# Performance work log

Measured on AMD Instinct MI355X. Metric: run time of the kernel, lower is better.

Reference implementation:

```python
import jax, jax.numpy as jnp
import numpy as np

N_EMBD = 2048
N_HEAD = 16
HEAD_DIM = N_EMBD // N_HEAD
MAX_SEQ = 2048
ROPE_BASE = 10000.0


def _build_rope_cache(seq_len, head_dim, base):
    theta = 1.0 / (base ** (jnp.arange(0, head_dim, 2, dtype=jnp.float32) / head_dim))
    idx_theta = jnp.arange(seq_len, dtype=jnp.float32)[:, None] * theta[None, :]  # [T, hd/2]
    return jnp.cos(idx_theta), jnp.sin(idx_theta)


def _apply_rope(x, cos, sin):
    # x: [B, T, H, hd]; interleaved (even, odd) pairing along last dim
    B, T, H, hd = x.shape
    xf = x.astype(jnp.float32).reshape(B, T, H, hd // 2, 2)
    x0, x1 = xf[..., 0], xf[..., 1]
    c = cos[None, :T, None, :]
    s = sin[None, :T, None, :]
    out = jnp.stack([x0 * c - x1 * s, x1 * c + x0 * s], axis=-1)
    return out.reshape(B, T, H, hd).astype(x.dtype)


def setup_inputs() -> dict:
    key = jax.random.key(0)
    k1, k2, k3 = jax.random.split(key, 3)
    x = jax.random.normal(k1, (2, 2048, N_EMBD), dtype=jnp.float32)
    # torch Linear(D, 3D, bias=False): y = x @ W.T ; store as [D, 3D] for x @ W
    scale = 1.0 / np.sqrt(N_EMBD)
    w_attn = jax.random.normal(k2, (N_EMBD, 3 * N_EMBD), dtype=jnp.float32) * scale
    w_proj = jax.random.normal(k3, (N_EMBD, N_EMBD), dtype=jnp.float32) * scale
    return {"x": x, "w_attn": w_attn, "w_proj": w_proj}


def reference(x, w_attn, w_proj):
    B, T, D = x.shape
    cos, sin = _build_rope_cache(MAX_SEQ, HEAD_DIM, ROPE_BASE)
    qkv = x @ w_attn                                   # [B, T, 3D]
    q, k, v = jnp.split(qkv, 3, axis=-1)
    q = q.reshape(B, T, N_HEAD, HEAD_DIM)
    k = k.reshape(B, T, N_HEAD, HEAD_DIM)
    v = v.reshape(B, T, N_HEAD, HEAD_DIM)
    q = _apply_rope(q, cos, sin)
    k = _apply_rope(k, cos, sin)
    # non-causal SDPA (original calls F.sdpa without is_causal)
    scale = 1.0 / jnp.sqrt(jnp.asarray(HEAD_DIM, dtype=q.dtype))
    scores = jnp.einsum("bqhd,bkhd->bhqk", q, k) * scale
    attn = jax.nn.softmax(scores, axis=-1)
    y = jnp.einsum("bhqk,bkhd->bqhd", attn, v).reshape(B, T, D)
    return y @ w_proj
```

## Files before the change

kernel.cpp:

```cpp
#include <hip/hip_runtime.h>
#include <cstdint>
#include <cstddef>

typedef __attribute__((ext_vector_type(8))) short bf16x8;
typedef __attribute__((ext_vector_type(8))) unsigned short us8;
typedef __attribute__((ext_vector_type(4))) float f32x4;

#define TSEQ 2048

__device__ __forceinline__ unsigned short f2bf(float f) {
  union { float f; uint32_t u; } v; v.f = f;
  uint32_t u = v.u;
  uint32_t r = (u + 0x7FFFu + ((u >> 16) & 1u)) >> 16;
  return (unsigned short)r;
}
__device__ __forceinline__ unsigned short f2bf_trunc(float f) {
  union { float f; uint32_t u; } v; v.f = f;
  return (unsigned short)(v.u >> 16);
}
__device__ __forceinline__ float bf2f(unsigned short h) {
  union { uint32_t u; float f; } v; v.u = ((uint32_t)h) << 16;
  return v.f;
}

__device__ __forceinline__ void async16(const void* g, void* l) {
  __builtin_amdgcn_global_load_lds(
      (const __attribute__((address_space(1))) unsigned int*)g,
      (__attribute__((address_space(3))) unsigned int*)l,
      16, 0, 0);
}

__global__ __launch_bounds__(256) void cvt_x(
    const float* __restrict__ in, unsigned short* __restrict__ out)
{
  const size_t i = ((size_t)blockIdx.x * 256 + threadIdx.x) * 16;
  f32x4 a0 = *(const f32x4*)(in + i);
  f32x4 a1 = *(const f32x4*)(in + i + 4);
  f32x4 a2 = *(const f32x4*)(in + i + 8);
  f32x4 a3 = *(const f32x4*)(in + i + 12);
  us8 lo, hi;
#pragma unroll
  for (int j = 0; j < 4; j++) {
    lo[j] = f2bf(a0[j]); lo[j + 4] = f2bf(a1[j]);
    hi[j] = f2bf(a2[j]); hi[j + 4] = f2bf(a3[j]);
  }
  *(us8*)(out + i) = lo;
  *(us8*)(out + i + 8) = hi;
}

__global__ __launch_bounds__(256) void transpose_w(
    const float* __restrict__ in, unsigned short* __restrict__ out,
    int R, int C)
{
  __shared__ unsigned short tile[32][33];
  const int bx = blockIdx.x * 32;
  const int by = blockIdx.y * 32;
  const int tx = threadIdx.x & 31;
  const int ty = threadIdx.x >> 5;
#pragma unroll
  for (int r = ty; r < 32; r += 8)
    tile[r][tx] = f2bf(in[(size_t)(by + r) * C + bx + tx]);
  __syncthreads();
#pragma unroll
  for (int r = ty; r < 32; r += 8)
    out[(size_t)(bx + r) * R + by + tx] = tile[tx][r];
}

template <int CF32>
__global__ __launch_bounds__(256) void gemm_bt(
    const unsigned short* __restrict__ A,
    const unsigned short* __restrict__ Bt,
    void* __restrict__ Cv,
    int M, int N, int K, int ldc)
{
  __shared__ unsigned short As[2][128 * 32];
  __shared__ unsigned short Bs[2][128 * 32];
  const int tid  = threadIdx.x;
  const int lane = tid & 63;
  const int w    = tid >> 6;
  const int m0   = blockIdx.y * 128;
  const int n0   = blockIdx.x * 128;
  const int wm   = (w & 1) * 64;
  const int wn   = (w >> 1) * 64;

  const int srow = lane >> 2;
  const int scol = (lane & 3) * 8;
  const unsigned short* ga0 = A  + (size_t)(m0 + w * 16 + srow) * K + scol;
  const unsigned short* ga1 = ga0 + (size_t)64 * K;
  const unsigned short* gb0 = Bt + (size_t)(n0 + w * 16 + srow) * K + scol;
  const unsigned short* gb1 = gb0 + (size_t)64 * K;

  f32x4 acc[4][4];
#pragma unroll
  for (int i = 0; i < 4; i++)
#pragma unroll
    for (int j = 0; j < 4; j++) acc[i][j] = (f32x4){0.f, 0.f, 0.f, 0.f};

  const int frow = lane & 15;
  const int fcol = (lane >> 4) * 8;

  for (int kt = 0; kt < K; kt += 64) {
    __syncthreads();
    async16(ga0 + kt,      &As[0][w * 512]);
    async16(ga1 + kt,      &As[0][(4 + w) * 512]);
    async16(ga0 + kt + 32, &As[1][w * 512]);
    async16(ga1 + kt + 32, &As[1][(4 + w) * 512]);
    async16(gb0 + kt,      &Bs[0][w * 512]);
    async16(gb1 + kt,      &Bs[0][(4 + w) * 512]);
    async16(gb0 + kt + 32, &Bs[1][w * 512]);
    async16(gb1 + kt + 32, &Bs[1][(4 + w) * 512]);
    __syncthreads();

#pragma unroll
    for (int h = 0; h < 2; h++) {
      bf16x8 af[4], bfr[4];
#pragma unroll
      for (int i = 0; i < 4; i++)
        af[i] = *(const bf16x8*)&As[h][(wm + i * 16 + frow) * 32 + fcol];
#pragma unroll
      for (int i = 0; i < 4; i++)
        bfr[i] = *(const bf16x8*)&Bs[h][(wn + i * 16 + frow) * 32 + fcol];
#pragma unroll
      for (int mi = 0; mi < 4; mi++)
#pragma unroll
        for (int ni = 0; ni < 4; ni++)
          acc[mi][ni] = __builtin_amdgcn_mfma_f32_16x16x32_bf16(
              af[mi], bfr[ni], acc[mi][ni], 0, 0, 0);
    }
  }

  const int crow0 = m0 + wm + (lane >> 4) * 4;
  const int ccol0 = n0 + wn + (lane & 15);
  if (CF32) {
    float* Cf = (float*)Cv;
#pragma unroll
    for (int mi = 0; mi < 4; mi++)
#pragma unroll
      for (int i = 0; i < 4; i++) {
        const int row = crow0 + mi * 16 + i;
#pragma unroll
        for (int ni = 0; ni < 4; ni++)
          Cf[(size_t)row * ldc + ccol0 + ni * 16] = acc[mi][ni][i];
      }
  } else {
    unsigned short* Cb = (unsigned short*)Cv;
#pragma unroll
    for (int mi = 0; mi < 4; mi++)
#pragma unroll
      for (int i = 0; i < 4; i++) {
        const int row = crow0 + mi * 16 + i;
#pragma unroll
        for (int ni = 0; ni < 4; ni++)
          Cb[(size_t)row * ldc + ccol0 + ni * 16] = f2bf(acc[mi][ni][i]);
      }
  }
}

__device__ __forceinline__ void stage8(
    const unsigned short* gA, const unsigned short* gB,
    unsigned short* asb, unsigned short* bsb, int K, int kt, int lw)
{
#pragma unroll
  for (int j = 0; j < 4; j++)
    async16(gA + (size_t)j * 64 * K + (size_t)kt * 64, asb + j * 4096 + lw);
#pragma unroll
  for (int j = 0; j < 4; j++)
    async16(gB + (size_t)j * 64 * K + (size_t)kt * 64, bsb + j * 4096 + lw);
}

__global__ __launch_bounds__(512, 2) void gemm256(
    const unsigned short* __restrict__ A,
    const unsigned short* __restrict__ Bt,
    unsigned short* __restrict__ C,
    int K, int ldc, int ntiles, int nwg)
{
  __shared__ unsigned short As[2][256 * 64];
  __shared__ unsigned short Bs[2][256 * 64];

  int wg = blockIdx.x;
  wg = (wg & 7) * (nwg >> 3) + (wg >> 3);
  const int m0 = (wg / ntiles) * 256;
  const int n0 = (wg % ntiles) * 256;

  const int tid  = threadIdx.x;
  const int lane = tid & 63;
  const int w    = tid >> 6;
  const int wr   = w & 1;
  const int wc   = w >> 1;

  const int srow  = tid >> 3;
  const int sslot = (tid ^ srow) & 7;
  const unsigned short* gA = A  + (size_t)(m0 + srow) * K + sslot * 8;
  const unsigned short* gB = Bt + (size_t)(n0 + srow) * K + sslot * 8;
  const int lw = w * 512;

  f32x4 acc[8][4];
#pragma unroll
  for (int i = 0; i < 8; i++)
#pragma unroll
    for (int j = 0; j < 4; j++) acc[i][j] = (f32x4){0.f, 0.f, 0.f, 0.f};

  const int frow = lane & 15;
  const int fq16 = (lane >> 4) * 16;
  const int axr  = (frow & 7) << 4;
  const int arow = (wr * 128 + frow) * 128;
  const int brow = (wc * 64 + frow) * 128;

#define RDA(buf, mi, kh) \
  (*(const bf16x8*)((const char*)&As[buf][0] + ((arow + (mi) * 2048 + (kh) * 64 + fq16) ^ axr)))
#define RDB(buf, ni, kh) \
  (*(const bf16x8*)((const char*)&Bs[buf][0] + ((brow + (ni) * 2048 + (kh) * 64 + fq16) ^ axr)))
#define STG_A(c, kt2) async16(gA + (size_t)(c) * 64 * K + (size_t)(kt2) * 64, &As[p][(c) * 4096 + lw])
#define STG_B(c, kt2) async16(gB + (size_t)(c) * 64 * K + (size_t)(kt2) * 64, &Bs[p][(c) * 4096 + lw])

  stage8(gA, gB, &As[0][0], &Bs[0][0], K, 0, lw);
  stage8(gA, gB, &As[1][0], &Bs[1][0], K, 1, lw);
  asm volatile("s_waitcnt vmcnt(8)" ::: "memory");
  __builtin_amdgcn_s_barrier();

  const int NT = K >> 6;
  bf16x8 a[4][2], b[4][2];
  for (int kt = 0; kt < NT; ++kt) {
    const int p = kt & 1;
    const bool pf = (kt + 2 < NT);

#pragma unroll
    for (int mi = 0; mi < 4; mi++) { a[mi][0] = RDA(p, mi, 0); a[mi][1] = RDA(p, mi, 1); }
#pragma unroll
    for (int ni = 0; ni < 2; ni++) { b[ni][0] = RDB(p, ni, 0); b[ni][1] = RDB(p, ni, 1); }
    __builtin_amdgcn_s_barrier();
    asm volatile("s_waitcnt lgkmcnt(0)" ::: "memory");
    __builtin_amdgcn_s_setprio(1);
#pragma unroll
    for (int mi = 0; mi < 4; mi++)
#pragma unroll
      for (int ni = 0; ni < 2; ni++)
#pragma unroll
        for (int kh = 0; kh < 2; kh++)
          acc[mi][ni] = __builtin_amdgcn_mfma_f32_16x16x32_bf16(
              a[mi][kh], b[ni][kh], acc[mi][ni], 0, 0, 0);
    __builtin_amdgcn_s_setprio(0);
    __builtin_amdgcn_s_barrier();

#pragma unroll
    for (int ni = 2; ni < 4; ni++) { b[ni][0] = RDB(p, ni, 0); b[ni][1] = RDB(p, ni, 1); }
    if (pf) { STG_A(0, kt + 2); STG_A(2, kt + 2); }
    __builtin_amdgcn_s_barrier();
    asm volatile("s_waitcnt lgkmcnt(0)" ::: "memory");
    __builtin_amdgcn_s_setprio(1);
#pragma unroll
    for (int mi = 0; mi < 4; mi++)
#pragma unroll
      for (int ni = 2; ni < 4; ni++)
#pragma unroll
        for (int kh = 0; kh < 2; kh++)
          acc[mi][ni] = __builtin_amdgcn_mfma_f32_16x16x32_bf16(
              a[mi][kh], b[ni][kh], acc[mi][ni], 0, 0, 0);
    __builtin_amdgcn_s_setprio(0);
    __builtin_amdgcn_s_barrier();

#pragma unroll
    for (int mi = 0; mi < 4; mi++) { a[mi][0] = RDA(p, mi + 4, 0); a[mi][1] = RDA(p, mi + 4, 1); }
    if (pf) { STG_B(0, kt + 2); STG_B(1, kt + 2); }
    __builtin_amdgcn_s_barrier();
    asm volatile("s_waitcnt lgkmcnt(0)" ::: "memory");
    __builtin_amdgcn_s_setprio(1);
#pragma unroll
    for (int mi = 0; mi < 4; mi++)
#pragma unroll
      for (int ni = 2; ni < 4; ni++)
#pragma unroll
        for (int kh = 0; kh < 2; kh++)
          acc[mi + 4][ni] = __builtin_amdgcn_mfma_f32_16x16x32_bf16(
              a[mi][kh], b[ni][kh], acc[mi + 4][ni], 0, 0, 0);
    __builtin_amdgcn_s_setprio(0);
    __builtin_amdgcn_s_barrier();

    if (pf) { STG_B(2, kt + 2); STG_B(3, kt + 2); STG_A(1, kt + 2); STG_A(3, kt + 2); }
    __builtin_amdgcn_s_setprio(1);
#pragma unroll
    for (int mi = 0; mi < 4; mi++)
#pragma unroll
      for (int ni = 0; ni < 2; ni++)
#pragma unroll
        for (int kh = 0; kh < 2; kh++)
          acc[mi + 4][ni] = __builtin_amdgcn_mfma_f32_16x16x32_bf16(
              a[mi][kh], b[ni][kh], acc[mi + 4][ni], 0, 0, 0);
    __builtin_amdgcn_s_setprio(0);
    if (pf) {
      asm volatile("s_waitcnt vmcnt(8)" ::: "memory");
    } else {
      asm volatile("s_waitcnt vmcnt(0)" ::: "memory");
    }
    __builtin_amdgcn_s_barrier();
  }
#undef RDA
#undef RDB
#undef STG_A
#undef STG_B

  const int crow0 = m0 + wr * 128 + (lane >> 4) * 4;
  const int ccol0 = n0 + wc * 64 + frow;
#pragma unroll
  for (int mi = 0; mi < 8; mi++)
#pragma unroll
    for (int i = 0; i < 4; i++) {
      const size_t row = (size_t)(crow0 + mi * 16 + i);
#pragma unroll
      for (int ni = 0; ni < 4; ni++)
        C[row * ldc + ccol0 + ni * 16] = f2bf(acc[mi][ni][i]);
    }
}

__global__ __launch_bounds__(256) void rope_qk(unsigned short* __restrict__ qkv)
{
  const int p   = blockIdx.x * 256 + threadIdx.x;
  const int row = p >> 11;
  const int col = (p & 2047) * 2;
  const int t   = row & (TSEQ - 1);
  const int hd  = col & 127;
  const float theta = exp2f((float)hd * -0.1038102531f);
  const float ang   = (float)t * theta;
  float s, c;
  sincosf(ang, &s, &c);
  const float sc = (col < 2048) ? 0.08838834764831845f : 1.0f;
  uint32_t* ptr = (uint32_t*)(qkv + (size_t)row * 6144 + col);
  const uint32_t u = *ptr;
  const float x0 = bf2f((unsigned short)(u & 0xffffu));
  const float x1 = bf2f((unsigned short)(u >> 16));
  const float o0 = (x0 * c - x1 * s) * sc;
  const float o1 = (x1 * c + x0 * s) * sc;
  *ptr = (uint32_t)f2bf(o0) | ((uint32_t)f2bf(o1) << 16);
}

__global__ __launch_bounds__(256) void repack_v(
    const unsigned short* __restrict__ qkv, unsigned short* __restrict__ Vtg)
{
  __shared__ unsigned short tile[32][33];
  const int tt = blockIdx.x * 32;
  const int dd = blockIdx.y * 32;
  const int bh = blockIdx.z;
  const int b  = bh >> 4, h = bh & 15;
  const int tx = threadIdx.x & 31;
  const int ty = threadIdx.x >> 5;
#pragma unroll
  for (int r = ty; r < 32; r += 8)
    tile[r][tx] = qkv[(size_t)(b * TSEQ + tt + r) * 6144 + 4096 + h * 128 + dd + tx];
  __syncthreads();
#pragma unroll
  for (int r = ty; r < 32; r += 8)
    Vtg[(size_t)bh * 262144 + (size_t)(dd + r) * TSEQ + tt + tx] = tile[tx][r];
}

__global__ __launch_bounds__(256) void attn(
    const unsigned short* __restrict__ qkv,
    const unsigned short* __restrict__ Vtg,
    unsigned short* __restrict__ y)
{
  __shared__ unsigned short Ks[64 * 136];
  __shared__ unsigned short Vs[144 * 72];
  __shared__ unsigned short Ps[4][32 * 72];

  const int tid  = threadIdx.x;
  const int lane = tid & 63;
  const int w    = tid >> 6;
  const int q0   = blockIdx.x * 128;
  const int h    = blockIdx.y;
  const int b    = blockIdx.z;
  const int bh   = b * 16 + h;
  const int quad = lane >> 4;
  const int l15  = lane & 15;
  const int kq   = quad * 8;

  for (int idx = tid; idx < 16 * 72; idx += 256)
    Vs[128 * 72 + idx] = (idx < 72) ? (unsigned short)0x3F80 : (unsigned short)0;

  bf16x8 qa[2][4];
#pragma unroll
  for (int mt = 0; mt < 2; mt++) {
    const unsigned short* gQ =
        qkv + (size_t)(b * TSEQ + q0 + w * 32 + mt * 16 + l15) * 6144 + h * 128 + kq;
#pragma unroll
    for (int dc = 0; dc < 4; dc++) qa[mt][dc] = *(const bf16x8*)(gQ + dc * 32);
  }

  f32x4 ot[2][9];
#pragma unroll
  for (int mt = 0; mt < 2; mt++)
#pragma unroll
    for (int nt = 0; nt < 9; nt++) ot[mt][nt] = (f32x4){0.f, 0.f, 0.f, 0.f};

  const int krow = tid >> 2;
  const int kd   = (tid & 3) * 32;
  const unsigned short* gK = qkv + (size_t)(b * TSEQ) * 6144 + 2048 + h * 128 + kd;
  const int vd = tid >> 1;
  const int vc = (tid & 1) * 32;
  const unsigned short* gVt = Vtg + (size_t)bh * 262144 + (size_t)vd * TSEQ + vc;

  for (int kb = 0; kb < TSEQ; kb += 64) {
    __syncthreads();
    {
      const unsigned short* pk = gK + (size_t)(kb + krow) * 6144;
#pragma unroll
      for (int j = 0; j < 4; j++)
        *(us8*)&Ks[krow * 136 + kd + j * 8] = *(const us8*)(pk + j * 8);
      const unsigned short* pv = gVt + kb;
#pragma unroll
      for (int j = 0; j < 4; j++)
        *(us8*)&Vs[vd * 72 + vc + j * 8] = *(const us8*)(pv + j * 8);
    }
    __syncthreads();

    f32x4 s[2][4];
#pragma unroll
    for (int mt = 0; mt < 2; mt++)
#pragma unroll
      for (int ct = 0; ct < 4; ct++) s[mt][ct] = (f32x4){0.f, 0.f, 0.f, 0.f};
#pragma unroll
    for (int dc = 0; dc < 4; dc++) {
#pragma unroll
      for (int ct = 0; ct < 4; ct++) {
        bf16x8 kf = *(const bf16x8*)&Ks[(ct * 16 + l15) * 136 + dc * 32 + kq];
        s[0][ct] = __builtin_amdgcn_mfma_f32_16x16x32_bf16(qa[0][dc], kf, s[0][ct], 0, 0, 0);
        s[1][ct] = __builtin_amdgcn_mfma_f32_16x16x32_bf16(qa[1][dc], kf, s[1][ct], 0, 0, 0);
      }
    }

    unsigned short* pw = &Ps[w][0];
#pragma unroll
    for (int mt = 0; mt < 2; mt++)
#pragma unroll
      for (int ct = 0; ct < 4; ct++)
#pragma unroll
        for (int i = 0; i < 4; i++)
          pw[(mt * 16 + quad * 4 + i) * 72 + ct * 16 + l15] =
              f2bf_trunc(__expf(fminf(s[mt][ct][i], 30.f)));

    __asm__ volatile("s_waitcnt lgkmcnt(0)" ::: "memory");

#pragma unroll
    for (int kc = 0; kc < 2; kc++) {
      bf16x8 pa0 = *(const bf16x8*)&pw[(l15) * 72 + kc * 32 + kq];
      bf16x8 pa1 = *(const bf16x8*)&pw[(16 + l15) * 72 + kc * 32 + kq];
#pragma unroll
      for (int nt = 0; nt < 9; nt++) {
        bf16x8 vb = *(const bf16x8*)&Vs[(nt * 16 + l15) * 72 + kc * 32 + kq];
        ot[0][nt] = __builtin_amdgcn_mfma_f32_16x16x32_bf16(pa0, vb, ot[0][nt], 0, 0, 0);
        ot[1][nt] = __builtin_amdgcn_mfma_f32_16x16x32_bf16(pa1, vb, ot[1][nt], 0, 0, 0);
      }
    }
  }

#pragma unroll
  for (int mt = 0; mt < 2; mt++) {
    unsigned short* gy =
        y + (size_t)(b * TSEQ + q0 + w * 32 + mt * 16 + quad * 4) * 2048 + h * 128 + l15;
#pragma unroll
    for (int i = 0; i < 4; i++) {
      const float inv = 1.0f / __shfl(ot[mt][8][i], lane & 48);
#pragma unroll
      for (int nt = 0; nt < 8; nt++)
        gy[(size_t)i * 2048 + nt * 16] = f2bf(ot[mt][nt][i] * inv);
    }
  }
}

extern "C" void kernel_launch(void* const* d_in, const int* in_sizes, int n_in,
                              void* d_out, int out_size, void* d_ws, size_t ws_size,
                              hipStream_t stream)
{
  const float* x      = (const float*)d_in[0];
  const float* w_attn = (const float*)d_in[1];
  const float* w_proj = (const float*)d_in[2];

  if (ws_size < 67108864u) return;

  char* ws = (char*)d_ws;
  unsigned short* qkv = (unsigned short*)(ws);
  unsigned short* xb  = (unsigned short*)(ws + 50331648);
  unsigned short* y   = xb;
  unsigned short* wT2 = (unsigned short*)(ws);
  unsigned short* wTa = (unsigned short*)d_out;
  unsigned short* Vtg = (unsigned short*)d_out;

  transpose_w<<<dim3(192, 64), 256, 0, stream>>>(w_attn, wTa, 2048, 6144);
  cvt_x<<<dim3(2048), 256, 0, stream>>>(x, xb);
  gemm256<<<dim3(384), 512, 0, stream>>>(xb, wTa, qkv, 2048, 6144, 24, 384);
  rope_qk<<<dim3(32768), 256, 0, stream>>>(qkv);
  repack_v<<<dim3(64, 4, 32), 256, 0, stream>>>(qkv, Vtg);
  attn<<<dim3(16, 16, 2), 256, 0, stream>>>(qkv, Vtg, y);
  transpose_w<<<dim3(64, 64), 256, 0, stream>>>(w_proj, wT2, 2048, 2048);
  gemm_bt<1><<<dim3(16, 32), 256, 0, stream>>>(y, wT2, d_out, 4096, 2048, 2048, 2048);
}
```

Before: 445.7 us.

## Software-pipeline LDS fragment reads across GEMM MFMA phases with split register sets

New measurement: 609.1 us. 36.7% more time.

```diff
diff --git a/kernel.cpp b/kernel.cpp
--- a/kernel.cpp
+++ b/kernel.cpp
@@ -29,6 +29,8 @@
       (__attribute__((address_space(3))) unsigned int*)l,
       16, 0, 0);
 }
+
+#define FENCE asm volatile("" ::: "memory")
 
 __global__ __launch_bounds__(256) void cvt_x(
     const float* __restrict__ in, unsigned short* __restrict__ out)
@@ -217,19 +219,23 @@
   stage8(gA, gB, &As[1][0], &Bs[1][0], K, 1, lw);
   asm volatile("s_waitcnt vmcnt(8)" ::: "memory");
   __builtin_amdgcn_s_barrier();
+  FENCE;
 
   const int NT = K >> 6;
-  bf16x8 a[4][2], b[4][2];
+  bf16x8 a0[4][2], a4[4][2], b0[2][2], b2[2][2];
+
+#pragma unroll
+  for (int mi = 0; mi < 4; mi++) { a0[mi][0] = RDA(0, mi, 0); a0[mi][1] = RDA(0, mi, 1); }
+#pragma unroll
+  for (int ni = 0; ni < 2; ni++) { b0[ni][0] = RDB(0, ni, 0); b0[ni][1] = RDB(0, ni, 1); }
+
   for (int kt = 0; kt < NT; ++kt) {
     const int p = kt & 1;
-    const bool pf = (kt + 2 < NT);
-
-#pragma unroll
-    for (int mi = 0; mi < 4; mi++) { a[mi][0] = RDA(p, mi, 0); a[mi][1] = RDA(p, mi, 1); }
-#pragma unroll
-    for (int ni = 0; ni < 2; ni++) { b[ni][0] = RDB(p, ni, 0); b[ni][1] = RDB(p, ni, 1); }
-    __builtin_amdgcn_s_barrier();
-    asm volatile("s_waitcnt lgkmcnt(0)" ::: "memory");
+
+#pragma unroll
+    for (int ni = 0; ni < 2; ni++) { b2[ni][0] = RDB(p, ni + 2, 0); b2[ni][1] = RDB(p, ni + 2, 1); }
+    asm volatile("s_waitcnt lgkmcnt(4)" ::: "memory");
+    __builtin_amdgcn_sched_barrier(0);
     __builtin_amdgcn_s_setprio(1);
 #pragma unroll
     for (int mi = 0; mi < 4; mi++)
@@ -238,61 +244,71 @@
 #pragma unroll
         for (int kh = 0; kh < 2; kh++)
           acc[mi][ni] = __builtin_amdgcn_mfma_f32_16x16x32_bf16(
-              a[mi][kh], b[ni][kh], acc[mi][ni], 0, 0, 0);
+              a0[mi][kh], b0[ni][kh], acc[mi][ni], 0, 0, 0);
     __builtin_amdgcn_s_setprio(0);
     __builtin_amdgcn_s_barrier();
-
-#pragma unroll
-    for (int ni = 2; ni < 4; ni++) { b[ni][0] = RDB(p, ni, 0); b[ni][1] = RDB(p, ni, 1); }
-    if (pf) { STG_A(0, kt + 2); STG_A(2, kt + 2); }
-    __builtin_amdgcn_s_barrier();
-    asm volatile("s_waitcnt lgkmcnt(0)" ::: "memory");
+    FENCE;
+
+    if (kt + 2 < NT) { STG_A(0, kt + 2); STG_A(2, kt + 2); }
+#pragma unroll
+    for (int mi = 0; mi < 4; mi++) { a4[mi][0] = RDA(p, mi + 4, 0); a4[mi][1] = RDA(p, mi + 4, 1); }
+    asm volatile("s_waitcnt lgkmcnt(8)" ::: "memory");
+    __builtin_amdgcn_sched_barrier(0);
     __builtin_amdgcn_s_setprio(1);
 #pragma unroll
     for (int mi = 0; mi < 4; mi++)
 #pragma unroll
-      for (int ni = 2; ni < 4; ni++)
+      for (int ni = 0; ni < 2; ni++)
 #pragma unroll
         for (int kh = 0; kh < 2; kh++)
-          acc[mi][ni] = __builtin_amdgcn_mfma_f32_16x16x32_bf16(
-              a[mi][kh], b[ni][kh], acc[mi][ni], 0, 0, 0);
+          acc[mi][ni + 2] = __builtin_amdgcn_mfma_f32_16x16x32_bf16(
+              a0[mi][kh], b2[ni][kh], acc[mi][ni + 2], 0, 0, 0);
     __builtin_amdgcn_s_setprio(0);
     __builtin_amdgcn_s_barrier();
-
-#pragma unroll
-    for (int mi = 0; mi < 4; mi++) { a[mi][0] = RDA(p, mi + 4, 0); a[mi][1] = RDA(p, mi + 4, 1); }
-    if (pf) { STG_B(0, kt + 2); STG_B(1, kt + 2); }
-    __builtin_amdgcn_s_barrier();
+    FENCE;
+
+    if (kt + 2 < NT) { STG_B(0, kt + 2); STG_B(1, kt + 2); }
     asm volatile("s_waitcnt lgkmcnt(0)" ::: "memory");
+    __builtin_amdgcn_sched_barrier(0);
     __builtin_amdgcn_s_setprio(1);
 #pragma unroll
     for (int mi = 0; mi < 4; mi++)
 #pragma unroll
-      for (int ni = 2; ni < 4; ni++)
+      for (int ni = 0; ni < 2; ni++)
 #pragma unroll
         for (int kh = 0; kh < 2; kh++)
           acc[mi + 4][ni] = __builtin_amdgcn_mfma_f32_16x16x32_bf16(
-              a[mi][kh], b[ni][kh], acc[mi + 4][ni], 0, 0, 0);
+              a4[mi][kh], b0[ni][kh], acc[mi + 4][ni], 0, 0, 0);
     __builtin_amdgcn_s_setprio(0);
     __builtin_amdgcn_s_barrier();
-
-    if (pf) { STG_B(2, kt + 2); STG_B(3, kt + 2); STG_A(1, kt + 2); STG_A(3, kt + 2); }
-    __builtin_amdgcn_s_setprio(1);
-#pragma unroll
-    for (int mi = 0; mi < 4; mi++)
-#pragma unroll
-      for (int ni = 0; ni < 2; ni++)
-#pragma unroll
-        for (int kh = 0; kh < 2; kh++)
-          acc[mi + 4][ni] = __builtin_amdgcn_mfma_f32_16x16x32_bf16(
-              a[mi][kh], b[ni][kh], acc[mi + 4][ni], 0, 0, 0);
-    __builtin_amdgcn_s_setprio(0);
-    if (pf) {
+    FENCE;
+
+    if (kt + 2 < NT) {
+      STG_B(2, kt + 2); STG_B(3, kt + 2); STG_A(1, kt + 2); STG_A(3, kt + 2);
       asm volatile("s_waitcnt vmcnt(8)" ::: "memory");
     } else {
       asm volatile("s_waitcnt vmcnt(0)" ::: "memory");
     }
     __builtin_amdgcn_s_barrier();
+    FENCE;
+    if (kt + 1 < NT) {
+      const int pn = p ^ 1;
+#pragma unroll
+      for (int mi = 0; mi < 4; mi++) { a0[mi][0] = RDA(pn, mi, 0); a0[mi][1] = RDA(pn, mi, 1); }
+#pragma unroll
+      for (int ni = 0; ni < 2; ni++) { b0[ni][0] = RDB(pn, ni, 0); b0[ni][1] = RDB(pn, ni, 1); }
+    }
+    __builtin_amdgcn_sched_barrier(0);
+    __builtin_amdgcn_s_setprio(1);
+#pragma unroll
+    for (int mi = 0; mi < 4; mi++)
+#pragma unroll
+      for (int ni = 0; ni < 2; ni++)
+#pragma unroll
+        for (int kh = 0; kh < 2; kh++)
+          acc[mi + 4][ni + 2] = __builtin_amdgcn_mfma_f32_16x16x32_bf16(
+              a4[mi][kh], b2[ni][kh], acc[mi + 4][ni + 2], 0, 0, 0);
+    __builtin_amdgcn_s_setprio(0);
   }
 #undef RDA
 #undef RDB
```
